# Optimization experiments

Hardware: AMD Instinct MI355X
Metric: run time of the kernel (lower is better)

## Reference

```python
import jax, jax.numpy as jnp
import numpy as np

ALPHA = 0.2
NEG = -9e15
EPS = 1e-5


def _gat(h, adj, W, a, out_features):
    # h: [B,N,Fin], adj: [B,N,N], W: [Fin,Fout], a: [2*Fout,1]
    Wh = jnp.matmul(h, W)                      # [B,N,Fout]
    Wh1 = jnp.matmul(Wh, a[:out_features])     # [B,N,1]
    Wh2 = jnp.matmul(Wh, a[out_features:])     # [B,N,1]
    e = Wh1 + jnp.swapaxes(Wh2, 1, 2)          # [B,N,N]
    e = jax.nn.leaky_relu(e, negative_slope=ALPHA)
    scores = jnp.where(adj > 0, e, NEG)
    att = jax.nn.softmax(scores, axis=1)       # NOTE: dim=1 as in source
    return jnp.matmul(att, Wh)                 # [B,N,Fout]


def _layernorm(x, g, b):
    mu = jnp.mean(x, axis=-1, keepdims=True)
    var = jnp.var(x, axis=-1, keepdims=True)
    return (x - mu) * jax.lax.rsqrt(var + EPS) * g + b


def setup_inputs() -> dict:
    key = jax.random.key(0)
    ks = jax.random.split(key, 8)
    B, N, F, H = 2, 4096, 256, 1024
    x = jax.random.normal(ks[0], (B, N, F), dtype=jnp.float32)
    adj = jax.random.randint(ks[1], (B, N, N), 0, 2, dtype=jnp.int32)
    def xavier(k, shape):
        fan_in, fan_out = shape[0], shape[1]
        lim = np.sqrt(6.0 / (fan_in + fan_out))
        return jax.random.uniform(k, shape, jnp.float32, -lim, lim)
    return {
        "x": x,
        "adj": adj,
        "W1": xavier(ks[2], (F, F)),
        "a1": xavier(ks[3], (2 * F, 1)),
        "W2": xavier(ks[4], (F, F)),
        "a2": xavier(ks[5], (2 * F, 1)),
        "w_ff1": xavier(ks[6], (F, H)) ,
        "b_ff1": jnp.zeros((H,), jnp.float32),
        "w_ff2": xavier(ks[7], (H, F)),
        "b_ff2": jnp.zeros((F,), jnp.float32),
        "g_ln1": jnp.ones((F,), jnp.float32),
        "b_ln1": jnp.zeros((F,), jnp.float32),
        "g_ln2": jnp.ones((F,), jnp.float32),
        "b_ln2": jnp.zeros((F,), jnp.float32),
    }


def reference(x, adj, W1, a1, W2, a2, w_ff1, b_ff1, w_ff2, b_ff2,
              g_ln1, b_ln1, g_ln2, b_ln2):
    Fout = W1.shape[1]
    residual = x
    # dropout is a no-op in eval mode
    h = _gat(x, adj, W1, a1, Fout)          # single head -> cat is identity
    h = _gat(h, adj, W2, a2, W2.shape[1])
    h = _layernorm(residual + h, g_ln1, b_ln1)
    residual2 = h
    ff = jnp.matmul(jax.nn.relu(jnp.matmul(h, w_ff1) + b_ff1), w_ff2) + b_ff2
    return _layernorm(residual2 + ff, g_ln2, b_ln2)
```

## Files before the change

kernel.cpp:

```cpp
#include <hip/hip_runtime.h>
#include <math.h>

#define ALPHA 0.2f
#define NEGV  -9e15f
#define EPSV  1e-5f

constexpr int B_ = 2, N_ = 4096, F_ = 256, H_ = 1024;
constexpr int SPLIT_ = 16;
constexpr int SPLITJ_ = 4;

typedef __attribute__((ext_vector_type(4))) float f32x4;
typedef __attribute__((ext_vector_type(8))) short s16x8;

__device__ __forceinline__ unsigned short f2bf(float f) {
    unsigned u = __builtin_bit_cast(unsigned, f);
    u += 0x7fffu + ((u >> 16) & 1u);
    return (unsigned short)(u >> 16);
}

__global__ __launch_bounds__(256) void zero_kernel(float* __restrict__ p)
{
    const int i = (blockIdx.x * 256 + threadIdx.x) * 4;
    *(float4*)&p[i] = make_float4(0.f, 0.f, 0.f, 0.f);
}

__global__ __launch_bounds__(256) void transp_all_kernel(
    const float* __restrict__ W1, const float* __restrict__ W2,
    const float* __restrict__ F1s, const float* __restrict__ F2s,
    unsigned short* __restrict__ D1, unsigned short* __restrict__ D2,
    unsigned short* __restrict__ D3, unsigned short* __restrict__ D4)
{
    const int mi = blockIdx.z;
    const float* src; unsigned short* dst; int R, Cc;
    if (mi == 0)      { src = W1;  dst = D1; R = 256;  Cc = 256; }
    else if (mi == 1) { src = W2;  dst = D2; R = 256;  Cc = 256; }
    else if (mi == 2) { src = F1s; dst = D3; R = 256;  Cc = 1024; }
    else              { src = F2s; dst = D4; R = 1024; Cc = 256; }
    const int r0 = blockIdx.x * 64, c0 = blockIdx.y * 64;
    if (r0 >= R || c0 >= Cc) return;

    __shared__ float T[64][65];
    const int t = threadIdx.x;
    #pragma unroll
    for (int s = 0; s < 4; ++s) {
        const int rr = s * 16 + (t >> 4);
        const int cq = t & 15;
        const float4 v = *(const float4*)&src[(size_t)(r0 + rr) * Cc + c0 + cq * 4];
        T[rr][cq * 4 + 0] = v.x; T[rr][cq * 4 + 1] = v.y;
        T[rr][cq * 4 + 2] = v.z; T[rr][cq * 4 + 3] = v.w;
    }
    __syncthreads();
    #pragma unroll
    for (int s = 0; s < 4; ++s) {
        const int cr = s * 16 + (t >> 4);
        const int rq = t & 15;
        ushort4 o;
        o.x = f2bf(T[rq * 4 + 0][cr]);
        o.y = f2bf(T[rq * 4 + 1][cr]);
        o.z = f2bf(T[rq * 4 + 2][cr]);
        o.w = f2bf(T[rq * 4 + 3][cr]);
        *(ushort4*)&dst[(size_t)(c0 + cr) * R + r0 + rq * 4] = o;
    }
}

__global__ __launch_bounds__(256) void gemm128_kernel(
    const void* __restrict__ Ap, const unsigned short* __restrict__ Wt,
    const float* __restrict__ bias, void* __restrict__ Cp,
    unsigned short* __restrict__ Tout, const float* __restrict__ wha,
    float* __restrict__ Wh1, float* __restrict__ Wh2,
    int Nc, int K, int relu, int a_bf16, int c_mode)
{
    __shared__ unsigned short As[128 * 72];
    __shared__ unsigned short Bs[128 * 72];
    const int t = threadIdx.x;
    const int w = t >> 6, l = t & 63;
    const int quad = l >> 4, l15 = l & 15;
    const int wr = w & 1, wc = w >> 1;
    const int row0 = blockIdx.y * 128, col0 = blockIdx.x * 128;
    const int sr = t >> 1;
    const int sk = (t & 1) * 32;

    f32x4 acc[4][4];
    #pragma unroll
    for (int it = 0; it < 4; ++it)
        #pragma unroll
        for (int ft = 0; ft < 4; ++ft) acc[it][ft] = (f32x4)(0.f);

    for (int k0 = 0; k0 < K; k0 += 64) {
        if (a_bf16) {
            const unsigned short* ap =
                (const unsigned short*)Ap + (size_t)(row0 + sr) * K + k0 + sk;
            #pragma unroll
            for (int u = 0; u < 4; ++u)
                *(s16x8*)&As[sr * 72 + sk + u * 8] = *(const s16x8*)(ap + u * 8);
        } else {
            const float* ap = (const float*)Ap + (size_t)(row0 + sr) * K + k0 + sk;
            #pragma unroll
            for (int u = 0; u < 8; ++u) {
                const float4 v = *(const float4*)(ap + u * 4);
                ushort4 o;
                o.x = f2bf(v.x); o.y = f2bf(v.y); o.z = f2bf(v.z); o.w = f2bf(v.w);
                *(ushort4*)&As[sr * 72 + sk + u * 4] = o;
            }
        }
        {
            const unsigned short* bp = Wt + (size_t)(col0 + sr) * K + k0 + sk;
            #pragma unroll
            for (int u = 0; u < 4; ++u)
                *(s16x8*)&Bs[sr * 72 + sk + u * 8] = *(const s16x8*)(bp + u * 8);
        }
        __syncthreads();
        #pragma unroll
        for (int ks = 0; ks < 64; ks += 32) {
            s16x8 af[4], bf[4];
            #pragma unroll
            for (int it = 0; it < 4; ++it)
                af[it] = *(const s16x8*)&As[(wr * 64 + it * 16 + l15) * 72 + ks + quad * 8];
            #pragma unroll
            for (int ft = 0; ft < 4; ++ft)
                bf[ft] = *(const s16x8*)&Bs[(wc * 64 + ft * 16 + l15) * 72 + ks + quad * 8];
            #pragma unroll
            for (int ft = 0; ft < 4; ++ft)
                #pragma unroll
                for (int it = 0; it < 4; ++it)
                    acc[it][ft] = __builtin_amdgcn_mfma_f32_16x16x32_bf16(
                        af[it], bf[ft], acc[it][ft], 0, 0, 0);
        }
        __syncthreads();
    }

    if (c_mode) {
        #pragma unroll
        for (int ft = 0; ft < 4; ++ft) {
            const int col = col0 + wc * 64 + ft * 16 + l15;
            const float bv = bias ? bias[col] : 0.f;
            #pragma unroll
            for (int it = 0; it < 4; ++it) {
                const int rbase = row0 + wr * 64 + it * 16 + quad * 4;
                #pragma unroll
                for (int rr = 0; rr < 4; ++rr) {
                    float v = acc[it][ft][rr] + bv;
                    if (relu) v = fmaxf(v, 0.f);
                    if (c_mode == 2)
                        ((unsigned short*)Cp)[(size_t)(rbase + rr) * Nc + col] = f2bf(v);
                    else
                        ((float*)Cp)[(size_t)(rbase + rr) * Nc + col] = v;
                }
            }
        }
    }

    if (Tout) {
        const int bb = row0 >> 12;
        #pragma unroll
        for (int ft = 0; ft < 4; ++ft) {
            const int col = col0 + wc * 64 + ft * 16 + l15;
            #pragma unroll
            for (int it = 0; it < 4; ++it) {
                const int ibase = (row0 & (N_ - 1)) + wr * 64 + it * 16 + quad * 4;
                ushort4 o;
                o.x = f2bf(acc[it][ft][0]); o.y = f2bf(acc[it][ft][1]);
                o.z = f2bf(acc[it][ft][2]); o.w = f2bf(acc[it][ft][3]);
                *(ushort4*)&Tout[((size_t)bb * F_ + col) * N_ + ibase] = o;
            }
        }
    }

    if (wha) {
        float a1v[4], a2v[4];
        #pragma unroll
        for (int ft = 0; ft < 4; ++ft) {
            const int col = col0 + wc * 64 + ft * 16 + l15;
            a1v[ft] = wha[col];
            a2v[ft] = wha[F_ + col];
        }
        #pragma unroll
        for (int it = 0; it < 4; ++it)
            #pragma unroll
            for (int rr = 0; rr < 4; ++rr) {
                float s1 = 0.f, s2 = 0.f;
                #pragma unroll
                for (int ft = 0; ft < 4; ++ft) {
                    s1 += acc[it][ft][rr] * a1v[ft];
                    s2 += acc[it][ft][rr] * a2v[ft];
                }
                #pragma unroll
                for (int mkk = 1; mkk < 16; mkk <<= 1) {
                    s1 += __shfl_xor(s1, mkk);
                    s2 += __shfl_xor(s2, mkk);
                }
                if (l15 == 0) {
                    const int row = row0 + wr * 64 + it * 16 + quad * 4 + rr;
                    atomicAdd(&Wh1[row], s1);
                    atomicAdd(&Wh2[row], s2);
                }
            }
    }
}

__global__ __launch_bounds__(256) void colstats_adj_kernel(
    const int* __restrict__ adj, unsigned long long* __restrict__ maskOut,
    const float* __restrict__ Wh1, const float* __restrict__ Wh2,
    float* __restrict__ pM, float* __restrict__ pS)
{
    const int t = threadIdx.x;
    const int j = blockIdx.x * 256 + t;
    const int sp = blockIdx.y;
    const int b = blockIdx.z;
    const int i0 = sp * (N_ / SPLIT_);
    const int w = t >> 6, l = t & 63;
    const float w2 = Wh2[b * N_ + j];
    const float* __restrict__ w1p = Wh1 + b * N_ + i0;
    const int* __restrict__ ap = adj + ((size_t)b * N_ + i0) * N_ + j;

    float m = -3.4e38f, s = 0.f;
    for (int c = 0; c < N_ / SPLIT_; c += 8) {
        int v[8];
        #pragma unroll
        for (int u = 0; u < 8; ++u) v[u] = ap[(size_t)(c + u) * N_];
        float x[8];
        #pragma unroll
        for (int u = 0; u < 8; ++u) {
            const bool act = v[u] > 0;
            const unsigned long long bm = __ballot(act);
            if (l == 0)
                maskOut[((size_t)b * N_ + i0 + c + u) * (N_ / 64) + blockIdx.x * 4 + w] = bm;
            const float e0 = w1p[c + u] + w2;
            const float e = fmaxf(e0, ALPHA * e0);
            x[u] = act ? e : NEGV;
        }
        const float cm = fmaxf(fmaxf(fmaxf(x[0], x[1]), fmaxf(x[2], x[3])),
                               fmaxf(fmaxf(x[4], x[5]), fmaxf(x[6], x[7])));
        const float nm = fmaxf(m, cm);
        float cs = 0.f;
        #pragma unroll
        for (int u = 0; u < 8; ++u) cs += __expf(x[u] - nm);
        s = s * __expf(m - nm) + cs;
        m = nm;
    }
    pM[((size_t)b * SPLIT_ + sp) * N_ + j] = m;
    pS[((size_t)b * SPLIT_ + sp) * N_ + j] = s;
}

__global__ __launch_bounds__(256) void colstats3_kernel(
    const unsigned long long* __restrict__ mask,
    const float* __restrict__ Wh1, const float* __restrict__ Wh2,
    float* __restrict__ pM, float* __restrict__ pS)
{
    const int t = threadIdx.x;
    const int j = blockIdx.x * 256 + t;
    const int sp = blockIdx.y;
    const int b = blockIdx.z;
    const int i0 = sp * (N_ / SPLIT_);
    const int w = t >> 6;
    const int jbit = t & 63;
    const float w2 = Wh2[b * N_ + j];
    const unsigned long long* __restrict__ mbase =
        mask + ((size_t)b * N_ + i0) * (N_ / 64) + blockIdx.x * 4 + w;
    const float* __restrict__ w1p = Wh1 + b * N_ + i0;

    float m = -3.4e38f, s = 0.f;
    for (int c = 0; c < N_ / SPLIT_; c += 8) {
        float x[8];
        #pragma unroll
        for (int u = 0; u < 8; ++u) {
            const unsigned long long mw = mbase[(size_t)(c + u) * (N_ / 64)];
            const float e0 = w1p[c + u] + w2;
            const float e = fmaxf(e0, ALPHA * e0);
            x[u] = ((mw >> jbit) & 1ull) ? e : NEGV;
        }
        const float cm = fmaxf(fmaxf(fmaxf(x[0], x[1]), fmaxf(x[2], x[3])),
                               fmaxf(fmaxf(x[4], x[5]), fmaxf(x[6], x[7])));
        const float nm = fmaxf(m, cm);
        float cs = 0.f;
        #pragma unroll
        for (int u = 0; u < 8; ++u) cs += __expf(x[u] - nm);
        s = s * __expf(m - nm) + cs;
        m = nm;
    }
    pM[((size_t)b * SPLIT_ + sp) * N_ + j] = m;
    pS[((size_t)b * SPLIT_ + sp) * N_ + j] = s;
}

__global__ __launch_bounds__(256) void colfin2_kernel(
    const float* __restrict__ pM, const float* __restrict__ pS,
    float* __restrict__ Mo)
{
    const int j = blockIdx.x * 256 + threadIdx.x;
    const int b = blockIdx.y;
    float m = -3.4e38f;
    #pragma unroll
    for (int s = 0; s < SPLIT_; ++s)
        m = fmaxf(m, pM[((size_t)b * SPLIT_ + s) * N_ + j]);
    float sum = 0.f;
    #pragma unroll
    for (int s = 0; s < SPLIT_; ++s)
        sum += pS[((size_t)b * SPLIT_ + s) * N_ + j] *
               __expf(pM[((size_t)b * SPLIT_ + s) * N_ + j] - m);
    Mo[b * N_ + j] = m + logf(sum);
}

__global__ __launch_bounds__(256) void att_mfma3_kernel(
    const unsigned short* __restrict__ mask16, const unsigned short* __restrict__ Wht,
    const float* __restrict__ Wh1, const float* __restrict__ Wh2,
    const float* __restrict__ Mo, float* __restrict__ part)
{
    __shared__ unsigned short Bs[256 * 72];
    __shared__ unsigned short Ps[64 * 72];
    __shared__ float w2s[1024];
    __shared__ float mos[1024];

    const int t = threadIdx.x;
    const int w = t >> 6, l = t & 63;
    const int quad = l >> 4, l15 = l & 15;
    const int b = blockIdx.z;
    const int i0 = blockIdx.x * 64;
    const int sp = blockIdx.y;
    const int jbase = sp * (N_ / SPLITJ_);

    const int pi = t >> 2;
    const int pj4 = t & 3;
    const float w1i = Wh1[b * N_ + i0 + pi];
    const unsigned short* __restrict__ mrow =
        mask16 + ((size_t)b * N_ + i0 + pi) * (N_ / 16);
    const unsigned short* __restrict__ WhtB = Wht + (size_t)b * F_ * N_;

    {
        const float4 a = *(const float4*)&Wh2[b * N_ + jbase + t * 4];
        const float4 c = *(const float4*)&Mo[b * N_ + jbase + t * 4];
        *(float4*)&w2s[t * 4] = a;
        *(float4*)&mos[t * 4] = c;
    }

    f32x4 acc[4][4];
    #pragma unroll
    for (int it = 0; it < 4; ++it)
        #pragma unroll
        for (int ft = 0; ft < 4; ++ft) acc[it][ft] = (f32x4)(0.f);

    const int f0s = t >> 3;
    const int prt = (t & 7) * 8;
    s16x8 breg[8];
    {
        const int jb = jbase;
        #pragma unroll
        for (int s = 0; s < 8; ++s)
            breg[s] = *(const s16x8*)&WhtB[(size_t)(f0s + s * 32) * N_ + jb + prt];
    }
    unsigned short mb_cur = mrow[jbase / 16 + pj4];
    __syncthreads();

    constexpr int NITER = (N_ / SPLITJ_) / 64;
    for (int itr = 0; itr < NITER; ++itr) {
        const int jb = jbase + itr * 64;
        #pragma unroll
        for (int s = 0; s < 8; ++s)
            *(s16x8*)&Bs[(f0s + s * 32) * 72 + prt] = breg[s];
        {
            const unsigned mb = mb_cur;
            const int jl = itr * 64 + pj4 * 16;
            #pragma unroll
            for (int u4 = 0; u4 < 4; ++u4) {
                const float4 w2v = *(const float4*)&w2s[jl + u4 * 4];
                const float4 mov = *(const float4*)&mos[jl + u4 * 4];
                ushort4 o;
                unsigned short* op = &o.x;
                #pragma unroll
                for (int u = 0; u < 4; ++u) {
                    const float xw = w1i + (&w2v.x)[u];
                    const float e = fmaxf(xw, ALPHA * xw);
                    const float x2 = ((mb >> (u4 * 4 + u)) & 1u) ? e : NEGV;
                    op[u] = f2bf(__expf(x2 - (&mov.x)[u]));
                }
                *(ushort4*)&Ps[pi * 72 + pj4 * 16 + u4 * 4] = o;
            }
        }
        __syncthreads();
        if (itr + 1 < NITER) {
            const int jn = jb + 64;
            #pragma unroll
            for (int s = 0; s < 8; ++s)
                breg[s] = *(const s16x8*)&WhtB[(size_t)(f0s + s * 32) * N_ + jn + prt];
            mb_cur = mrow[jn / 16 + pj4];
        }
        #pragma unroll
        for (int ks = 0; ks < 64; ks += 32) {
            s16x8 af[4];
            #pragma unroll
            for (int it = 0; it < 4; ++it)
                af[it] = *(const s16x8*)&Ps[(it * 16 + l15) * 72 + ks + quad * 8];
            #pragma unroll
            for (int ft = 0; ft < 4; ++ft) {
                const s16x8 bf =
                    *(const s16x8*)&Bs[(w * 64 + ft * 16 + l15) * 72 + ks + quad * 8];
                #pragma unroll
                for (int it = 0; it < 4; ++it)
                    acc[it][ft] = __builtin_amdgcn_mfma_f32_16x16x32_bf16(
                        af[it], bf, acc[it][ft], 0, 0, 0);
            }
        }
        __syncthreads();
    }

    float* __restrict__ pout = part + ((size_t)sp * B_ + b) * N_ * F_;
    #pragma unroll
    for (int it = 0; it < 4; ++it)
        #pragma unroll
        for (int ft = 0; ft < 4; ++ft) {
            const int col = w * 64 + ft * 16 + l15;
            #pragma unroll
            for (int rr = 0; rr < 4; ++rr) {
                const int row = i0 + it * 16 + quad * 4 + rr;
                pout[(size_t)row * F_ + col] = acc[it][ft][rr];
            }
        }
}

__global__ __launch_bounds__(256) void reduce4b_kernel(
    const float* __restrict__ p, unsigned short* __restrict__ outb)
{
    const size_t i = ((size_t)blockIdx.x * 256 + threadIdx.x) * 4;
    const size_t S = (size_t)B_ * N_ * F_;
    const float4 a = *(const float4*)&p[i];
    const float4 b = *(const float4*)&p[i + S];
    const float4 c = *(const float4*)&p[i + 2 * S];
    const float4 d = *(const float4*)&p[i + 3 * S];
    ushort4 o;
    o.x = f2bf(a.x + b.x + c.x + d.x);
    o.y = f2bf(a.y + b.y + c.y + d.y);
    o.z = f2bf(a.z + b.z + c.z + d.z);
    o.w = f2bf(a.w + b.w + c.w + d.w);
    *(ushort4*)&outb[i] = o;
}

__global__ __launch_bounds__(256) void addln4_kernel(
    const float* __restrict__ X, const float* __restrict__ p,
    const float* __restrict__ g, const float* __restrict__ bta,
    float* __restrict__ outf, unsigned short* __restrict__ outb)
{
    const int row = blockIdx.x;
    const int t = threadIdx.x;
    const size_t idx = (size_t)row * F_ + t;
    const size_t S = (size_t)B_ * N_ * F_;
    const float v = X[idx] + p[idx] + p[idx + S] + p[idx + 2 * S] + p[idx + 3 * S];
    float s1 = v, s2 = v * v;
    #pragma unroll
    for (int off = 32; off > 0; off >>= 1) {
        s1 += __shfl_down(s1, off);
        s2 += __shfl_down(s2, off);
    }
    __shared__ float r1[4], r2[4];
    __shared__ float mu_s, rs_s;
    const int wid = t >> 6, lane = t & 63;
    if (lane == 0) { r1[wid] = s1; r2[wid] = s2; }
    __syncthreads();
    if (t == 0) {
        const float a = r1[0] + r1[1] + r1[2] + r1[3];
        const float q = r2[0] + r2[1] + r2[2] + r2[3];
        const float mu = a * (1.f / F_);
        const float var = q * (1.f / F_) - mu * mu;
        mu_s = mu;
        rs_s = rsqrtf(var + EPSV);
    }
    __syncthreads();
    const float r = (v - mu_s) * rs_s * g[t] + bta[t];
    outf[idx] = r;
    outb[idx] = f2bf(r);
}

__global__ __launch_bounds__(256) void addln_kernel(
    const float* __restrict__ X, const float* __restrict__ Y,
    const float* __restrict__ g, const float* __restrict__ bta,
    float* __restrict__ out)
{
    const int row = blockIdx.x;
    const int t = threadIdx.x;
    const size_t idx = (size_t)row * F_ + t;
    const float v = X[idx] + Y[idx];
    float s1 = v, s2 = v * v;
    #pragma unroll
    for (int off = 32; off > 0; off >>= 1) {
        s1 += __shfl_down(s1, off);
        s2 += __shfl_down(s2, off);
    }
    __shared__ float r1[4], r2[4];
    __shared__ float mu_s, rs_s;
    const int wid = t >> 6, lane = t & 63;
    if (lane == 0) { r1[wid] = s1; r2[wid] = s2; }
    __syncthreads();
    if (t == 0) {
        const float a = r1[0] + r1[1] + r1[2] + r1[3];
        const float q = r2[0] + r2[1] + r2[2] + r2[3];
        const float mu = a * (1.f / F_);
        const float var = q * (1.f / F_) - mu * mu;
        mu_s = mu;
        rs_s = rsqrtf(var + EPSV);
    }
    __syncthreads();
    out[idx] = (v - mu_s) * rs_s * g[t] + bta[t];
}

extern "C" void kernel_launch(void* const* d_in, const int* in_sizes, int n_in,
                              void* d_out, int out_size, void* d_ws, size_t ws_size,
                              hipStream_t stream)
{
    const float* x     = (const float*)d_in[0];
    const int*   adj   = (const int*)d_in[1];
    const float* W1    = (const float*)d_in[2];
    const float* a1    = (const float*)d_in[3];
    const float* W2    = (const float*)d_in[4];
    const float* a2    = (const float*)d_in[5];
    const float* w_ff1 = (const float*)d_in[6];
    const float* b_ff1 = (const float*)d_in[7];
    const float* w_ff2 = (const float*)d_in[8];
    const float* b_ff2 = (const float*)d_in[9];
    const float* g_ln1 = (const float*)d_in[10];
    const float* b_ln1 = (const float*)d_in[11];
    const float* g_ln2 = (const float*)d_in[12];
    const float* b_ln2 = (const float*)d_in[13];
    float* out = (float*)d_out;

    const int Rtot = B_ * N_;
    char* wsb = (char*)d_ws;
    float* part  = (float*)wsb;
    float* ln1   = (float*)(wsb + 33554432);
    float* ffout = (float*)(wsb + 41943040);
    unsigned short* mid  = (unsigned short*)(wsb + 50331648);
    unsigned short* ln1b = (unsigned short*)(wsb + 67108864);
    unsigned short* g1b  = (unsigned short*)(wsb + 71303168);
    unsigned short* Wht  = (unsigned short*)(wsb + 75497472);
    unsigned long long* mask = (unsigned long long*)(wsb + 79691776);
    unsigned short* mask16 = (unsigned short*)mask;
    unsigned short* Wt1  = (unsigned short*)(wsb + 83886080);
    unsigned short* Wt2  = Wt1 + 65536;
    unsigned short* Wtf1 = Wt2 + 65536;
    unsigned short* Wtf2 = Wtf1 + 262144;
    float* WhA1 = (float*)(wsb + 85196800);
    float* WhA2 = WhA1 + 8192;
    float* WhB1 = WhA2 + 8192;
    float* WhB2 = WhB1 + 8192;
    float* Mo   = (float*)(wsb + 85327872);
    float* pM   = (float*)(wsb + 85360640);
    float* pS   = (float*)(wsb + 85884928);

    const dim3 statsG(N_ / 256, SPLIT_, B_);
    const dim3 finG(N_ / 256, B_);
    const dim3 attG(N_ / 64, SPLITJ_, B_);

    zero_kernel<<<32, 256, 0, stream>>>(WhA1);
    transp_all_kernel<<<dim3(16, 16, 4), 256, 0, stream>>>(
        W1, W2, w_ff1, w_ff2, Wt1, Wt2, Wtf1, Wtf2);

    gemm128_kernel<<<dim3(2, 64), 256, 0, stream>>>(
        x, Wt1, nullptr, nullptr, Wht, a1, WhA1, WhA2, F_, F_, 0, 0, 0);
    colstats_adj_kernel<<<statsG, 256, 0, stream>>>(adj, mask, WhA1, WhA2, pM, pS);
    colfin2_kernel<<<finG, 256, 0, stream>>>(pM, pS, Mo);
    att_mfma3_kernel<<<attG, 256, 0, stream>>>(mask16, Wht, WhA1, WhA2, Mo, part);
    reduce4b_kernel<<<2048, 256, 0, stream>>>(part, g1b);

    gemm128_kernel<<<dim3(2, 64), 256, 0, stream>>>(
        g1b, Wt2, nullptr, nullptr, Wht, a2, WhB1, WhB2, F_, F_, 0, 1, 0);
    colstats3_kernel<<<statsG, 256, 0, stream>>>(mask, WhB1, WhB2, pM, pS);
    colfin2_kernel<<<finG, 256, 0, stream>>>(pM, pS, Mo);
    att_mfma3_kernel<<<attG, 256, 0, stream>>>(mask16, Wht, WhB1, WhB2, Mo, part);

    addln4_kernel<<<Rtot, 256, 0, stream>>>(x, part, g_ln1, b_ln1, ln1, ln1b);

    gemm128_kernel<<<dim3(8, 64), 256, 0, stream>>>(
        ln1b, Wtf1, b_ff1, mid, nullptr, nullptr, nullptr, nullptr, H_, F_, 1, 1, 2);
    gemm128_kernel<<<dim3(2, 64), 256, 0, stream>>>(
        mid, Wtf2, b_ff2, ffout, nullptr, nullptr, nullptr, nullptr, F_, H_, 0, 1, 1);

    addln_kernel<<<Rtot, 256, 0, stream>>>(ln1, ffout, g_ln2, b_ln2, out);
}
```

Measured before the change: 422.2 us.

## Double-buffer attention P tiles, load B directly to registers, add 64-row GEMM

The attention kernel now loads B fragments straight from global memory into registers in MFMA layout instead of staging them through shared memory. It double-buffers the probability tile so computing the next P overlaps the current MFMA step, and remaps block indices so batch and split are grouped per XCD, with launch bounds asking for two blocks per CU. A new 64-row GEMM kernel replaces the 128-row one for the N=256 output GEMMs, doubling the block count to fill more CUs. The risks are more register pressure and uncoalesced direct global B loads.

```diff
diff --git a/kernel.cpp b/kernel.cpp
--- a/kernel.cpp
+++ b/kernel.cpp
@@ -198,6 +198,137 @@
     }
 }
 
+__global__ __launch_bounds__(256) void gemm64_kernel(
+    const void* __restrict__ Ap, const unsigned short* __restrict__ Wt,
+    const float* __restrict__ bias, void* __restrict__ Cp,
+    unsigned short* __restrict__ Tout, const float* __restrict__ wha,
+    float* __restrict__ Wh1, float* __restrict__ Wh2,
+    int Nc, int K, int relu, int a_bf16, int c_mode)
+{
+    __shared__ unsigned short As[64 * 72];
+    __shared__ unsigned short Bs[128 * 72];
+    const int t = threadIdx.x;
+    const int w = t >> 6, l = t & 63;
+    const int quad = l >> 4, l15 = l & 15;
+    const int row0 = blockIdx.y * 64, col0 = blockIdx.x * 128;
+    const int sra = t >> 2;
+    const int ska = (t & 3) * 16;
+    const int srb = t >> 1;
+    const int skb = (t & 1) * 32;
+
+    f32x4 acc[4][2];
+    #pragma unroll
+    for (int it = 0; it < 4; ++it)
+        #pragma unroll
+        for (int ft = 0; ft < 2; ++ft) acc[it][ft] = (f32x4)(0.f);
+
+    for (int k0 = 0; k0 < K; k0 += 64) {
+        if (a_bf16) {
+            const unsigned short* ap =
+                (const unsigned short*)Ap + (size_t)(row0 + sra) * K + k0 + ska;
+            *(s16x8*)&As[sra * 72 + ska]     = *(const s16x8*)ap;
+            *(s16x8*)&As[sra * 72 + ska + 8] = *(const s16x8*)(ap + 8);
+        } else {
+            const float* ap = (const float*)Ap + (size_t)(row0 + sra) * K + k0 + ska;
+            #pragma unroll
+            for (int u = 0; u < 4; ++u) {
+                const float4 v = *(const float4*)(ap + u * 4);
+                ushort4 o;
+                o.x = f2bf(v.x); o.y = f2bf(v.y); o.z = f2bf(v.z); o.w = f2bf(v.w);
+                *(ushort4*)&As[sra * 72 + ska + u * 4] = o;
+            }
+        }
+        {
+            const unsigned short* bp = Wt + (size_t)(col0 + srb) * K + k0 + skb;
+            #pragma unroll
+            for (int u = 0; u < 4; ++u)
+                *(s16x8*)&Bs[srb * 72 + skb + u * 8] = *(const s16x8*)(bp + u * 8);
+        }
+        __syncthreads();
+        #pragma unroll
+        for (int ks = 0; ks < 64; ks += 32) {
+            s16x8 af[4], bf[2];
+            #pragma unroll
+            for (int it = 0; it < 4; ++it)
+                af[it] = *(const s16x8*)&As[(it * 16 + l15) * 72 + ks + quad * 8];
+            #pragma unroll
+            for (int ft = 0; ft < 2; ++ft)
+                bf[ft] = *(const s16x8*)&Bs[(w * 32 + ft * 16 + l15) * 72 + ks + quad * 8];
+            #pragma unroll
+            for (int ft = 0; ft < 2; ++ft)
+                #pragma unroll
+                for (int it = 0; it < 4; ++it)
+                    acc[it][ft] = __builtin_amdgcn_mfma_f32_16x16x32_bf16(
+                        af[it], bf[ft], acc[it][ft], 0, 0, 0);
+        }
+        __syncthreads();
+    }
+
+    if (c_mode) {
+        #pragma unroll
+        for (int ft = 0; ft < 2; ++ft) {
+            const int col = col0 + w * 32 + ft * 16 + l15;
+            const float bv = bias ? bias[col] : 0.f;
+            #pragma unroll
+            for (int it = 0; it < 4; ++it) {
+                const int rbase = row0 + it * 16 + quad * 4;
+                #pragma unroll
+                for (int rr = 0; rr < 4; ++rr) {
+                    float v = acc[it][ft][rr] + bv;
+                    if (relu) v = fmaxf(v, 0.f);
+                    if (c_mode == 2)
+                        ((unsigned short*)Cp)[(size_t)(rbase + rr) * Nc + col] = f2bf(v);
+                    else
+                        ((float*)Cp)[(size_t)(rbase + rr) * Nc + col] = v;
+                }
+            }
+        }
+    }
+
+    if (Tout) {
+        const int bb = row0 >> 12;
+        #pragma unroll
+        for (int ft = 0; ft < 2; ++ft) {
+            const int col = col0 + w * 32 + ft * 16 + l15;
+            #pragma unroll
+            for (int it = 0; it < 4; ++it) {
+                const int ibase = (row0 & (N_ - 1)) + it * 16 + quad * 4;
+                ushort4 o;
+                o.x = f2bf(acc[it][ft][0]); o.y = f2bf(acc[it][ft][1]);
+                o.z = f2bf(acc[it][ft][2]); o.w = f2bf(acc[it][ft][3]);
+                *(ushort4*)&Tout[((size_t)bb * F_ + col) * N_ + ibase] = o;
+            }
+        }
+    }
+
+    if (wha) {
+        float a1v[2], a2v[2];
+        #pragma unroll
+        for (int ft = 0; ft < 2; ++ft) {
+            const int col = col0 + w * 32 + ft * 16 + l15;
+            a1v[ft] = wha[col];
+            a2v[ft] = wha[F_ + col];
+        }
+        #pragma unroll
+        for (int it = 0; it < 4; ++it)
+            #pragma unroll
+            for (int rr = 0; rr < 4; ++rr) {
+                float s1 = acc[it][0][rr] * a1v[0] + acc[it][1][rr] * a1v[1];
+                float s2 = acc[it][0][rr] * a2v[0] + acc[it][1][rr] * a2v[1];
+                #pragma unroll
+                for (int mkk = 1; mkk < 16; mkk <<= 1) {
+                    s1 += __shfl_xor(s1, mkk);
+                    s2 += __shfl_xor(s2, mkk);
+                }
+                if (l15 == 0) {
+                    const int row = row0 + it * 16 + quad * 4 + rr;
+                    atomicAdd(&Wh1[row], s1);
+                    atomicAdd(&Wh2[row], s2);
+                }
+            }
+    }
+}
+
 __global__ __launch_bounds__(256) void colstats_adj_kernel(
     const int* __restrict__ adj, unsigned long long* __restrict__ maskOut,
     const float* __restrict__ Wh1, const float* __restrict__ Wh2,
@@ -300,29 +431,31 @@
     Mo[b * N_ + j] = m + logf(sum);
 }
 
-__global__ __launch_bounds__(256) void att_mfma3_kernel(
+__global__ __launch_bounds__(256, 2) void att_mfma4_kernel(
     const unsigned short* __restrict__ mask16, const unsigned short* __restrict__ Wht,
     const float* __restrict__ Wh1, const float* __restrict__ Wh2,
     const float* __restrict__ Mo, float* __restrict__ part)
 {
-    __shared__ unsigned short Bs[256 * 72];
-    __shared__ unsigned short Ps[64 * 72];
+    __shared__ unsigned short Ps[2][64 * 72];
     __shared__ float w2s[1024];
     __shared__ float mos[1024];
 
     const int t = threadIdx.x;
     const int w = t >> 6, l = t & 63;
     const int quad = l >> 4, l15 = l & 15;
-    const int b = blockIdx.z;
-    const int i0 = blockIdx.x * 64;
-    const int sp = blockIdx.y;
+
+    const int lin = blockIdx.x + (blockIdx.y << 6) + (blockIdx.z << 8);
+    const int xcd = lin & 7;
+    const int b = xcd >> 2;
+    const int sp = xcd & 3;
+    const int i0 = (lin >> 3) << 6;
     const int jbase = sp * (N_ / SPLITJ_);
 
     const int pi = t >> 2;
     const int pj4 = t & 3;
     const float w1i = Wh1[b * N_ + i0 + pi];
     const unsigned short* __restrict__ mrow =
-        mask16 + ((size_t)b * N_ + i0 + pi) * (N_ / 16);
+        mask16 + ((size_t)b * N_ + i0 + pi) * (N_ / 16) + pj4;
     const unsigned short* __restrict__ WhtB = Wht + (size_t)b * F_ * N_;
 
     {
@@ -338,67 +471,74 @@
         #pragma unroll
         for (int ft = 0; ft < 4; ++ft) acc[it][ft] = (f32x4)(0.f);
 
-    const int f0s = t >> 3;
-    const int prt = (t & 7) * 8;
-    s16x8 breg[8];
-    {
-        const int jb = jbase;
-        #pragma unroll
-        for (int s = 0; s < 8; ++s)
-            breg[s] = *(const s16x8*)&WhtB[(size_t)(f0s + s * 32) * N_ + jb + prt];
-    }
-    unsigned short mb_cur = mrow[jbase / 16 + pj4];
-    __syncthreads();
-
-    constexpr int NITER = (N_ / SPLITJ_) / 64;
-    for (int itr = 0; itr < NITER; ++itr) {
-        const int jb = jbase + itr * 64;
-        #pragma unroll
-        for (int s = 0; s < 8; ++s)
-            *(s16x8*)&Bs[(f0s + s * 32) * 72 + prt] = breg[s];
-        {
-            const unsigned mb = mb_cur;
-            const int jl = itr * 64 + pj4 * 16;
-            #pragma unroll
-            for (int u4 = 0; u4 < 4; ++u4) {
-                const float4 w2v = *(const float4*)&w2s[jl + u4 * 4];
-                const float4 mov = *(const float4*)&mos[jl + u4 * 4];
-                ushort4 o;
-                unsigned short* op = &o.x;
-                #pragma unroll
-                for (int u = 0; u < 4; ++u) {
-                    const float xw = w1i + (&w2v.x)[u];
-                    const float e = fmaxf(xw, ALPHA * xw);
-                    const float x2 = ((mb >> (u4 * 4 + u)) & 1u) ? e : NEGV;
-                    op[u] = f2bf(__expf(x2 - (&mov.x)[u]));
-                }
-                *(ushort4*)&Ps[pi * 72 + pj4 * 16 + u4 * 4] = o;
-            }
-        }
-        __syncthreads();
-        if (itr + 1 < NITER) {
-            const int jn = jb + 64;
-            #pragma unroll
-            for (int s = 0; s < 8; ++s)
-                breg[s] = *(const s16x8*)&WhtB[(size_t)(f0s + s * 32) * N_ + jn + prt];
-            mb_cur = mrow[jn / 16 + pj4];
-        }
-        #pragma unroll
-        for (int ks = 0; ks < 64; ks += 32) {
+    const unsigned short* __restrict__ bbase =
+        WhtB + (size_t)(w * 64 + l15) * N_ + jbase + quad * 8;
+
+    s16x8 bA[8], bB[8];
+
+    auto prefB = [&](int itr2, s16x8* dst) {
+        const unsigned short* nb = bbase + itr2 * 64;
+        #pragma unroll
+        for (int ft = 0; ft < 4; ++ft)
+            #pragma unroll
+            for (int kk = 0; kk < 2; ++kk)
+                dst[ft * 2 + kk] = *(const s16x8*)&nb[(size_t)ft * 16 * N_ + kk * 32];
+    };
+
+    auto computeP = [&](int itr2, unsigned short* psdst) {
+        const int jl = itr2 * 64 + pj4 * 16;
+        const unsigned mb = mrow[(jbase >> 4) + itr2 * 4];
+        s16x8 o0, o1;
+        #pragma unroll
+        for (int u4 = 0; u4 < 4; ++u4) {
+            const float4 w2v = *(const float4*)&w2s[jl + u4 * 4];
+            const float4 mov = *(const float4*)&mos[jl + u4 * 4];
+            #pragma unroll
+            for (int u = 0; u < 4; ++u) {
+                const float xw = w1i + (&w2v.x)[u];
+                const float e = fmaxf(xw, ALPHA * xw);
+                const float x2 = ((mb >> (u4 * 4 + u)) & 1u) ? e : NEGV;
+                const short pv = (short)f2bf(__expf(x2 - (&mov.x)[u]));
+                if (u4 < 2) o0[u4 * 4 + u] = pv;
+                else        o1[(u4 - 2) * 4 + u] = pv;
+            }
+        }
+        *(s16x8*)&psdst[pi * 72 + pj4 * 16]     = o0;
+        *(s16x8*)&psdst[pi * 72 + pj4 * 16 + 8] = o1;
+    };
+
+    auto mfmaStep = [&](const unsigned short* ps, const s16x8* breg) {
+        #pragma unroll
+        for (int ksidx = 0; ksidx < 2; ++ksidx) {
             s16x8 af[4];
             #pragma unroll
             for (int it = 0; it < 4; ++it)
-                af[it] = *(const s16x8*)&Ps[(it * 16 + l15) * 72 + ks + quad * 8];
-            #pragma unroll
-            for (int ft = 0; ft < 4; ++ft) {
-                const s16x8 bf =
-                    *(const s16x8*)&Bs[(w * 64 + ft * 16 + l15) * 72 + ks + quad * 8];
+                af[it] = *(const s16x8*)&ps[(it * 16 + l15) * 72 + ksidx * 32 + quad * 8];
+            #pragma unroll
+            for (int ft = 0; ft < 4; ++ft)
                 #pragma unroll
                 for (int it = 0; it < 4; ++it)
                     acc[it][ft] = __builtin_amdgcn_mfma_f32_16x16x32_bf16(
-                        af[it], bf, acc[it][ft], 0, 0, 0);
-            }
-        }
+                        af[it], breg[ft * 2 + ksidx], acc[it][ft], 0, 0, 0);
+        }
+    };
+
+    prefB(0, bA);
+    __syncthreads();
+    computeP(0, &Ps[0][0]);
+    __syncthreads();
+
+    constexpr int NITER = (N_ / SPLITJ_) / 64;
+    for (int itr = 0; itr < NITER; itr += 2) {
+        prefB(itr + 1, bB);
+        computeP(itr + 1, &Ps[1][0]);
+        mfmaStep(&Ps[0][0], bA);
+        __syncthreads();
+        if (itr + 2 < NITER) {
+            prefB(itr + 2, bA);
+            computeP(itr + 2, &Ps[0][0]);
+        }
+        mfmaStep(&Ps[1][0], bB);
         __syncthreads();
     }
 
@@ -551,24 +691,24 @@
     transp_all_kernel<<<dim3(16, 16, 4), 256, 0, stream>>>(
         W1, W2, w_ff1, w_ff2, Wt1, Wt2, Wtf1, Wtf2);
 
-    gemm128_kernel<<<dim3(2, 64), 256, 0, stream>>>(
+    gemm64_kernel<<<dim3(2, 128), 256, 0, stream>>>(
         x, Wt1, nullptr, nullptr, Wht, a1, WhA1, WhA2, F_, F_, 0, 0, 0);
     colstats_adj_kernel<<<statsG, 256, 0, stream>>>(adj, mask, WhA1, WhA2, pM, pS);
     colfin2_kernel<<<finG, 256, 0, stream>>>(pM, pS, Mo);
-    att_mfma3_kernel<<<attG, 256, 0, stream>>>(mask16, Wht, WhA1, WhA2, Mo, part);
+    att_mfma4_kernel<<<attG, 256, 0, stream>>>(mask16, Wht, WhA1, WhA2, Mo, part);
     reduce4b_kernel<<<2048, 256, 0, stream>>>(part, g1b);
 
-    gemm128_kernel<<<dim3(2, 64), 256, 0, stream>>>(
+    gemm64_kernel<<<dim3(2, 128), 256, 0, stream>>>(
         g1b, Wt2, nullptr, nullptr, Wht, a2, WhB1, WhB2, F_, F_, 0, 1, 0);
     colstats3_kernel<<<statsG, 256, 0, stream>>>(mask, WhB1, WhB2, pM, pS);
     colfin2_kernel<<<finG, 256, 0, stream>>>(pM, pS, Mo);
-    att_mfma3_kernel<<<attG, 256, 0, stream>>>(mask16, Wht, WhB1, WhB2, Mo, part);
+    att_mfma4_kernel<<<attG, 256, 0, stream>>>(mask16, Wht, WhB1, WhB2, Mo, part);
 
     addln4_kernel<<<Rtot, 256, 0, stream>>>(x, part, g_ln1, b_ln1, ln1, ln1b);
 
     gemm128_kernel<<<dim3(8, 64), 256, 0, stream>>>(
         ln1b, Wtf1, b_ff1, mid, nullptr, nullptr, nullptr, nullptr, H_, F_, 1, 1, 2);
-    gemm128_kernel<<<dim3(2, 64), 256, 0, stream>>>(
+    gemm64_kernel<<<dim3(2, 128), 256, 0, stream>>>(
         mid, Wtf2, b_ff2, ffout, nullptr, nullptr, nullptr, nullptr, F_, H_, 0, 1, 1);
 
     addln_kernel<<<Rtot, 256, 0, stream>>>(ln1, ffout, g_ln2, b_ln2, out);
```

New measurement: 424.0 us. About the same (+0.4%).
